# Kernel tuning notes

Hardware: AMD Instinct MI355X
Metric: run time of the kernel (lower is better)

Reference implementation:

```python
import jax, jax.numpy as jnp
import numpy as np

DIM = 1024
HEADS = 16
DIM_HEAD = 64
INNER = HEADS * DIM_HEAD  # 1024
SCALE = DIM_HEAD ** -0.5


def setup_inputs() -> dict:
    key = jax.random.key(0)
    k1, k2, k3, k4 = jax.random.split(key, 4)
    B, N = 2, 2048
    x = jax.random.normal(k1, (B, N, DIM), dtype=jnp.float32)
    # to_qkv: Linear(dim, 3*inner_dim, bias=False); weight stored as [out, in] in torch,
    # here as [in, out] for x @ W.
    w_qkv = jax.random.normal(k2, (DIM, 3 * INNER), dtype=jnp.float32) * (DIM ** -0.5)
    # to_out: Linear(inner_dim, dim) with bias
    w_out = jax.random.normal(k3, (INNER, DIM), dtype=jnp.float32) * (INNER ** -0.5)
    b_out = jax.random.normal(k4, (DIM,), dtype=jnp.float32) * 0.02
    return {"x": x, "w_qkv": w_qkv, "w_out": w_out, "b_out": b_out}


def reference(x, w_qkv, w_out, b_out):
    B, N, _ = x.shape
    qkv = x @ w_qkv                                  # [B, N, 3*INNER]
    q, k, v = jnp.split(qkv, 3, axis=-1)             # each [B, N, INNER]
    def to_heads(t):
        return t.reshape(B, N, HEADS, DIM_HEAD).transpose(0, 2, 1, 3)  # [B,H,N,D]
    q, k, v = to_heads(q), to_heads(k), to_heads(v)
    dots = jnp.einsum('bhnd,bhmd->bhnm', q, k) * SCALE  # [B,H,N,N]
    attn = jax.nn.softmax(dots, axis=-1)
    out = jnp.einsum('bhnm,bhmd->bhnd', attn, v)        # [B,H,N,D]
    out = out.transpose(0, 2, 1, 3).reshape(B, N, INNER)
    return out @ w_out + b_out
```

## Files before the change

### kernel.cpp

```cpp
#include <hip/hip_runtime.h>
#include <hip/hip_bf16.h>
#include <stdint.h>

#define PDIM   1024
#define HEADS  16
#define DHEAD  64
#define BATCH  2
#define SEQ    2048
#define ROWS   (BATCH*SEQ)
#define NBH    (BATCH*HEADS)

typedef __attribute__((ext_vector_type(8))) short s8v;
typedef __attribute__((ext_vector_type(4))) float f32x4;
typedef __attribute__((ext_vector_type(16))) float f32x16;
typedef unsigned short ushort_t;
typedef unsigned int   uint32;

#define QSCALE 0.18033688011112042f
#define MFIX 12.0f

__device__ __forceinline__ ushort_t f2bf(float x){
  union { float f; uint32 u; } v; v.f = x;
  uint32 r = v.u + 0x7FFFu + ((v.u >> 16) & 1u);
  return (ushort_t)(r >> 16);
}
__device__ __forceinline__ uint32 cvt_pk_bf16(float lo, float hi){
  uint32 r;
  asm("v_cvt_pk_bf16_f32 %0, %1, %2" : "=v"(r) : "v"(lo), "v"(hi));
  return r;
}

typedef const __attribute__((address_space(1))) void* gas_ptr;
typedef __attribute__((address_space(3))) void*       las_ptr;
__device__ __forceinline__ void g2l16(const void* g, void* l){
  __builtin_amdgcn_global_load_lds((gas_ptr)g, (las_ptr)l, 16, 0, 0);
}

__global__ __launch_bounds__(256) void k_prep(
    const float* __restrict__ x, const float* __restrict__ w_qkv,
    const float* __restrict__ w_out,
    ushort_t* __restrict__ Xh, ushort_t* __restrict__ Wqt_h,
    ushort_t* __restrict__ Wot_h){
  __shared__ float tile[64][65];
  const int bid = blockIdx.x;
  if (bid < 4096){
    int i = bid * 256 + threadIdx.x;
    float4 v = reinterpret_cast<const float4*>(x)[i];
    reinterpret_cast<ushort4*>(Xh)[i] =
        make_ushort4(f2bf(v.x), f2bf(v.y), f2bf(v.z), f2bf(v.w));
    return;
  }
  const float* src; ushort_t* dst; int R, C, cb, rb;
  if (bid < 4864){
    int t = bid - 4096; src = w_qkv; dst = Wqt_h; R = 1024; C = 3072;
    cb = (t % 48) * 64; rb = (t / 48) * 64;
  } else {
    int t = bid - 4864; src = w_out; dst = Wot_h; R = 1024; C = 1024;
    cb = (t % 16) * 64; rb = (t / 16) * 64;
  }
  int t = threadIdx.x;
  int lw = t >> 6, lc = t & 63;
#pragma unroll
  for (int i = 0; i < 16; i++){
    int r = i * 4 + lw;
    tile[r][lc] = src[(size_t)(rb + r) * C + cb + lc];
  }
  __syncthreads();
#pragma unroll
  for (int i = 0; i < 16; i++){
    int c = i * 4 + lw;
    dst[(size_t)(cb + c) * R + rb + lc] = f2bf(tile[lc][c]);
  }
}

#define GBM 128
#define GBN 128
#define GBK 64

__global__ __launch_bounds__(256, 2) void k_gemm_qkv(
    const ushort_t* __restrict__ Xh, const ushort_t* __restrict__ Wqt_h,
    ushort_t* __restrict__ Qh, ushort_t* __restrict__ Kh, ushort_t* __restrict__ Vth){
  __shared__ __align__(16) ushort_t Asm[2][GBM * GBK];
  __shared__ __align__(16) ushort_t Bsm[2][GBM * GBK];
  const int tid  = threadIdx.x;
  const int wave = tid >> 6, lane = tid & 63;
  const int mb = blockIdx.y * GBM, nb = blockIdx.x * GBN;
  const int wr = wave >> 1, wc = wave & 1;
  const int l15 = lane & 15, l4 = lane >> 4;
  const int rsub = lane >> 3;
  const int schunk = ((lane & 7) ^ rsub) * 8;
  f32x4 acc[4][4] = {};

  auto stage = [&](int buf, int kb){
    int k0 = kb * GBK;
#pragma unroll
    for (int i = 0; i < 4; i++){
      int row = (i * 4 + wave) * 8 + rsub;
      g2l16(Xh    + (size_t)(mb + row) * 1024 + k0 + schunk, &Asm[buf][(i * 4 + wave) * 512]);
      g2l16(Wqt_h + (size_t)(nb + row) * 1024 + k0 + schunk, &Bsm[buf][(i * 4 + wave) * 512]);
    }
  };

  stage(0, 0);

  for (int kb = 0; kb < 16; kb++){
    const int cur = kb & 1;
    if (kb < 15){
      stage(cur ^ 1, kb + 1);
      asm volatile("s_waitcnt vmcnt(8)" ::: "memory");
    } else {
      asm volatile("s_waitcnt vmcnt(0)" ::: "memory");
    }
    __builtin_amdgcn_s_barrier();
    __builtin_amdgcn_s_setprio(1);
#pragma unroll
    for (int ks = 0; ks < 2; ks++){
      s8v af[4], bfr[4];
#pragma unroll
      for (int f = 0; f < 4; f++){
        int ch = (((ks * 4 + l4) ^ (l15 & 7)) << 3);
        af[f]  = *reinterpret_cast<const s8v*>(&Asm[cur][(wr * 64 + f * 16 + l15) * 64 + ch]);
        bfr[f] = *reinterpret_cast<const s8v*>(&Bsm[cur][(wc * 64 + f * 16 + l15) * 64 + ch]);
      }
#pragma unroll
      for (int fr = 0; fr < 4; fr++)
#pragma unroll
        for (int fc = 0; fc < 4; fc++)
          acc[fr][fc] = __builtin_amdgcn_mfma_f32_16x16x32_bf16(af[fr], bfr[fc], acc[fr][fc], 0, 0, 0);
    }
    __builtin_amdgcn_s_setprio(0);
    __builtin_amdgcn_s_barrier();
  }

  const int pnum = nb >> 10;
#pragma unroll
  for (int fr = 0; fr < 4; fr++){
    int row  = mb + wr * 64 + fr * 16 + l4 * 4;
    int b    = row >> 11;
    int nseq = row & 2047;
#pragma unroll
    for (int fc = 0; fc < 4; fc++){
      int col = nb + wc * 64 + fc * 16 + l15;
      int rem = col & 1023;
      int h = rem >> 6, d = rem & 63;
      int bh = b * 16 + h;
      if (pnum == 0){
        size_t base = ((size_t)bh * SEQ + nseq) * 64 + d;
#pragma unroll
        for (int r = 0; r < 4; r++)
          Qh[base + (size_t)r * 64] = f2bf(acc[fr][fc][r] * QSCALE);
      } else if (pnum == 1){
        size_t base = ((size_t)bh * SEQ + nseq) * 64 + d;
#pragma unroll
        for (int r = 0; r < 4; r++)
          Kh[base + (size_t)r * 64] = f2bf(acc[fr][fc][r]);
      } else {
        size_t base = ((size_t)bh * 64 + d) * SEQ + nseq;
        *reinterpret_cast<ushort4*>(&Vth[base]) =
            make_ushort4(f2bf(acc[fr][fc][0]), f2bf(acc[fr][fc][1]),
                         f2bf(acc[fr][fc][2]), f2bf(acc[fr][fc][3]));
      }
    }
  }
}

__global__ __launch_bounds__(256, 2) void k_gemm_out(
    const ushort_t* __restrict__ Ah, const ushort_t* __restrict__ Bth,
    float* __restrict__ C, const float* __restrict__ bias){
  __shared__ __align__(16) ushort_t Asm[2][GBM * GBK];
  __shared__ __align__(16) ushort_t Bsm[2][GBM * GBK];
  const int tid  = threadIdx.x;
  const int wave = tid >> 6, lane = tid & 63;
  const int mb = blockIdx.y * GBM, nb = blockIdx.x * GBN;
  const int wr = wave >> 1, wc = wave & 1;
  const int l15 = lane & 15, l4 = lane >> 4;
  const int rsub = lane >> 3;
  const int schunk = ((lane & 7) ^ rsub) * 8;
  f32x4 acc[4][4] = {};

  auto stage = [&](int buf, int kb){
    int k0 = kb * GBK;
#pragma unroll
    for (int i = 0; i < 4; i++){
      int row = (i * 4 + wave) * 8 + rsub;
      g2l16(Ah  + (size_t)(mb + row) * 1024 + k0 + schunk, &Asm[buf][(i * 4 + wave) * 512]);
      g2l16(Bth + (size_t)(nb + row) * 1024 + k0 + schunk, &Bsm[buf][(i * 4 + wave) * 512]);
    }
  };

  stage(0, 0);

  for (int kb = 0; kb < 16; kb++){
    const int cur = kb & 1;
    if (kb < 15){
      stage(cur ^ 1, kb + 1);
      asm volatile("s_waitcnt vmcnt(8)" ::: "memory");
    } else {
      asm volatile("s_waitcnt vmcnt(0)" ::: "memory");
    }
    __builtin_amdgcn_s_barrier();
    __builtin_amdgcn_s_setprio(1);
#pragma unroll
    for (int ks = 0; ks < 2; ks++){
      s8v af[4], bfr[4];
#pragma unroll
      for (int f = 0; f < 4; f++){
        int ch = (((ks * 4 + l4) ^ (l15 & 7)) << 3);
        af[f]  = *reinterpret_cast<const s8v*>(&Asm[cur][(wr * 64 + f * 16 + l15) * 64 + ch]);
        bfr[f] = *reinterpret_cast<const s8v*>(&Bsm[cur][(wc * 64 + f * 16 + l15) * 64 + ch]);
      }
#pragma unroll
      for (int fr = 0; fr < 4; fr++)
#pragma unroll
        for (int fc = 0; fc < 4; fc++)
          acc[fr][fc] = __builtin_amdgcn_mfma_f32_16x16x32_bf16(af[fr], bfr[fc], acc[fr][fc], 0, 0, 0);
    }
    __builtin_amdgcn_s_setprio(0);
    __builtin_amdgcn_s_barrier();
  }
#pragma unroll
  for (int fr = 0; fr < 4; fr++){
    int row = mb + wr * 64 + fr * 16 + l4 * 4;
#pragma unroll
    for (int fc = 0; fc < 4; fc++){
      int col = nb + wc * 64 + fc * 16 + l15;
      float bv = bias[col];
#pragma unroll
      for (int r = 0; r < 4; r++)
        C[(size_t)(row + r) * 1024 + col] = acc[fr][fc][r] + bv;
    }
  }
}

__global__ __launch_bounds__(256, 2) void k_flash(
    const ushort_t* __restrict__ Qh, const ushort_t* __restrict__ Kh,
    const ushort_t* __restrict__ Vth, ushort_t* __restrict__ Ah){
  __shared__ __align__(16) ushort_t KhS[2][64 * 64];
  __shared__ __align__(16) ushort_t VhS[2][64 * 64];
  const int lid = blockIdx.x;
  const int xcd = lid & 7, g = lid >> 3;
  const int bh = xcd * 4 + (g & 3);
  const int qb = (g >> 2) * 128;
  const int tid = threadIdx.x, wave = tid >> 6, lane = tid & 63;
  const int l31 = lane & 31, hh = lane >> 5;
  const int b = bh >> 4, hd = bh & 15;
  const size_t hbase = (size_t)bh * SEQ * 64;
  const int rsub = lane >> 3;
  const int schunk = ((lane & 7) ^ rsub) * 8;

  int fch[4];
#pragma unroll
  for (int s = 0; s < 4; s++)
    fch[s] = (((2 * s + hh) ^ (l31 & 7)) << 3);
  const int fbase = l31 * 64;

  s8v qf[4];
#pragma unroll
  for (int s = 0; s < 4; s++)
    qf[s] = *reinterpret_cast<const s8v*>(
        &Qh[hbase + (size_t)(qb + wave * 32 + l31) * 64 + s * 16 + hh * 8]);

  f32x16 o0 = {}, o1 = {};
  float lsum = 0.f;

  auto stage = [&](int buf, int kt){
    int kvb = kt * 64;
#pragma unroll
    for (int i = 0; i < 2; i++){
      int row = (i * 4 + wave) * 8 + rsub;
      g2l16(Kh  + hbase + (size_t)(kvb + row) * 64 + schunk, &KhS[buf][(i * 4 + wave) * 512]);
      g2l16(Vth + ((size_t)bh * 64 + row) * SEQ + kvb + schunk, &VhS[buf][(i * 4 + wave) * 512]);
    }
  };

  stage(0, 0);

  for (int kt = 0; kt < 32; kt++){
    const int cur = kt & 1;
    if (kt < 31){
      stage(cur ^ 1, kt + 1);
      asm volatile("s_waitcnt vmcnt(4)" ::: "memory");
    } else {
      asm volatile("s_waitcnt vmcnt(0)" ::: "memory");
    }
    __builtin_amdgcn_s_barrier();

    f32x16 s0 = {}, s1 = {};
    __builtin_amdgcn_s_setprio(1);
#pragma unroll
    for (int s = 0; s < 4; s++){
      s8v kf0 = *reinterpret_cast<const s8v*>(&KhS[cur][fbase + fch[s]]);
      s8v kf1 = *reinterpret_cast<const s8v*>(&KhS[cur][fbase + 2048 + fch[s]]);
      s0 = __builtin_amdgcn_mfma_f32_32x32x16_bf16(kf0, qf[s], s0, 0, 0, 0);
      s1 = __builtin_amdgcn_mfma_f32_32x32x16_bf16(kf1, qf[s], s1, 0, 0, 0);
    }
    __builtin_amdgcn_s_setprio(0);

    uint32 w[2][8];
#pragma unroll
    for (int t = 0; t < 8; t++){
      float pa = __builtin_amdgcn_exp2f(s0[2 * t]     - MFIX);
      float pb = __builtin_amdgcn_exp2f(s0[2 * t + 1] - MFIX);
      lsum += pa + pb;
      w[0][t] = cvt_pk_bf16(pa, pb);
    }
#pragma unroll
    for (int t = 0; t < 8; t++){
      float pa = __builtin_amdgcn_exp2f(s1[2 * t]     - MFIX);
      float pb = __builtin_amdgcn_exp2f(s1[2 * t + 1] - MFIX);
      lsum += pa + pb;
      w[1][t] = cvt_pk_bf16(pa, pb);
    }

    __builtin_amdgcn_s_setprio(1);
#pragma unroll
    for (int s = 0; s < 4; s++){
      const int rb = s >> 1, u = (s & 1) * 4;
      uint32 m0 = w[rb][u],     m2 = w[rb][u + 2];
      uint32 m1 = w[rb][u + 1], m3 = w[rb][u + 3];
      asm("v_permlane32_swap_b32 %0, %1" : "+v"(m0), "+v"(m2));
      asm("v_permlane32_swap_b32 %0, %1" : "+v"(m1), "+v"(m3));
      union { uint32 u4[4]; s8v v; } pf;
      pf.u4[0] = m0; pf.u4[1] = m1; pf.u4[2] = m2; pf.u4[3] = m3;
      s8v vf0 = *reinterpret_cast<const s8v*>(&VhS[cur][fbase + fch[s]]);
      s8v vf1 = *reinterpret_cast<const s8v*>(&VhS[cur][fbase + 2048 + fch[s]]);
      o0 = __builtin_amdgcn_mfma_f32_32x32x16_bf16(pf.v, vf0, o0, 0, 0, 0);
      o1 = __builtin_amdgcn_mfma_f32_32x32x16_bf16(pf.v, vf1, o1, 0, 0, 0);
    }
    __builtin_amdgcn_s_setprio(0);
    __builtin_amdgcn_s_barrier();
  }

  lsum += __shfl_xor(lsum, 32);
  float linv = 1.f / lsum;
#pragma unroll
  for (int r = 0; r < 16; r++){
    int q = (r & 3) + 8 * (r >> 2) + 4 * hh;
    float sc = __shfl(linv, q);
    int n = qb + wave * 32 + q;
    size_t rowb = (size_t)(b * SEQ + n) * 1024 + hd * 64;
    Ah[rowb + l31]      = f2bf(o0[r] * sc);
    Ah[rowb + 32 + l31] = f2bf(o1[r] * sc);
  }
}

extern "C" void kernel_launch(void* const* d_in, const int* in_sizes, int n_in,
                              void* d_out, int out_size, void* d_ws, size_t ws_size,
                              hipStream_t stream){
  const float* x     = (const float*)d_in[0];
  const float* w_qkv = (const float*)d_in[1];
  const float* w_out = (const float*)d_in[2];
  const float* b_out = (const float*)d_in[3];
  float* out = (float*)d_out;
  char* ws = (char*)d_ws;

  ushort_t* Xh    = (ushort_t*)(ws);
  ushort_t* Wqt_h = (ushort_t*)(ws + 8388608);
  ushort_t* Wot_h = (ushort_t*)(ws + 14680064);
  ushort_t* Qh    = (ushort_t*)(ws + 16777216);
  ushort_t* Kh    = (ushort_t*)(ws + 25165824);
  ushort_t* Vth   = (ushort_t*)(ws + 33554432);
  ushort_t* Ah    = (ushort_t*)(ws + 41943040);

  k_prep<<<5120, 256, 0, stream>>>(x, w_qkv, w_out, Xh, Wqt_h, Wot_h);
  k_gemm_qkv<<<dim3(24, 32), 256, 0, stream>>>(Xh, Wqt_h, Qh, Kh, Vth);
  k_flash<<<512, 256, 0, stream>>>(Qh, Kh, Vth, Ah);
  k_gemm_out<<<dim3(8, 32), 256, 0, stream>>>(Ah, Wot_h, out, b_out);
}
```

Before: 115.7 us.

## Shrink flash tiles to 64 queries and 32 keys with 2-wave blocks

The flash-attention kernel now runs 2-wave blocks of 64 query rows and iterates over 32-key tiles (64 steps instead of 32). The grid doubles to 1024 blocks and LDS per block halves, allowing more resident blocks per CU. A new V-tile swizzle and pointer-increment staging are added. Separately, the Q softmax scale is folded into the transposed Q weights in the prep kernel instead of being applied in the QKV GEMM epilogue. The trade-off is more barriers and K/V loads per query row, which lowers data reuse.

```diff
diff --git a/kernel.cpp b/kernel.cpp
--- a/kernel.cpp
+++ b/kernel.cpp
@@ -51,9 +51,11 @@
     return;
   }
   const float* src; ushort_t* dst; int R, C, cb, rb;
+  float scl = 1.f;
   if (bid < 4864){
     int t = bid - 4096; src = w_qkv; dst = Wqt_h; R = 1024; C = 3072;
     cb = (t % 48) * 64; rb = (t / 48) * 64;
+    if (cb < 1024) scl = QSCALE;
   } else {
     int t = bid - 4864; src = w_out; dst = Wot_h; R = 1024; C = 1024;
     cb = (t % 16) * 64; rb = (t / 16) * 64;
@@ -69,7 +71,7 @@
 #pragma unroll
   for (int i = 0; i < 16; i++){
     int c = i * 4 + lw;
-    dst[(size_t)(cb + c) * R + rb + lc] = f2bf(tile[lc][c]);
+    dst[(size_t)(cb + c) * R + rb + lc] = f2bf(tile[lc][c] * scl);
   }
 }
 
@@ -148,7 +150,7 @@
         size_t base = ((size_t)bh * SEQ + nseq) * 64 + d;
 #pragma unroll
         for (int r = 0; r < 4; r++)
-          Qh[base + (size_t)r * 64] = f2bf(acc[fr][fc][r] * QSCALE);
+          Qh[base + (size_t)r * 64] = f2bf(acc[fr][fc][r]);
       } else if (pnum == 1){
         size_t base = ((size_t)bh * SEQ + nseq) * 64 + d;
 #pragma unroll
@@ -232,27 +234,30 @@
   }
 }
 
-__global__ __launch_bounds__(256, 2) void k_flash(
+__global__ __launch_bounds__(128, 4) void k_flash(
     const ushort_t* __restrict__ Qh, const ushort_t* __restrict__ Kh,
     const ushort_t* __restrict__ Vth, ushort_t* __restrict__ Ah){
-  __shared__ __align__(16) ushort_t KhS[2][64 * 64];
-  __shared__ __align__(16) ushort_t VhS[2][64 * 64];
+  __shared__ __align__(16) ushort_t KhS[2][32 * 64];
+  __shared__ __align__(16) ushort_t VhS[2][64 * 32];
   const int lid = blockIdx.x;
   const int xcd = lid & 7, g = lid >> 3;
   const int bh = xcd * 4 + (g & 3);
-  const int qb = (g >> 2) * 128;
+  const int qb = (g >> 2) * 64;
   const int tid = threadIdx.x, wave = tid >> 6, lane = tid & 63;
   const int l31 = lane & 31, hh = lane >> 5;
   const int b = bh >> 4, hd = bh & 15;
   const size_t hbase = (size_t)bh * SEQ * 64;
   const int rsub = lane >> 3;
-  const int schunk = ((lane & 7) ^ rsub) * 8;
-
-  int fch[4];
-#pragma unroll
-  for (int s = 0; s < 4; s++)
-    fch[s] = (((2 * s + hh) ^ (l31 & 7)) << 3);
-  const int fbase = l31 * 64;
+  const int schunkK = ((lane & 7) ^ rsub) * 8;
+  const int schunkV = ((lane & 3) ^ ((lane >> 2) & 3)) * 8;
+
+  int fchK[4], fchV[2];
+#pragma unroll
+  for (int s = 0; s < 4; s++) fchK[s] = (((2 * s + hh) ^ (l31 & 7)) << 3);
+#pragma unroll
+  for (int s = 0; s < 2; s++) fchV[s] = (((2 * s + hh) ^ (l31 & 3)) << 3);
+  const int fbK = l31 * 64;
+  const int fbV = l31 * 32;
 
   s8v qf[4];
 #pragma unroll
@@ -263,67 +268,60 @@
   f32x16 o0 = {}, o1 = {};
   float lsum = 0.f;
 
-  auto stage = [&](int buf, int kt){
-    int kvb = kt * 64;
-#pragma unroll
-    for (int i = 0; i < 2; i++){
-      int row = (i * 4 + wave) * 8 + rsub;
-      g2l16(Kh  + hbase + (size_t)(kvb + row) * 64 + schunk, &KhS[buf][(i * 4 + wave) * 512]);
-      g2l16(Vth + ((size_t)bh * 64 + row) * SEQ + kvb + schunk, &VhS[buf][(i * 4 + wave) * 512]);
-    }
+  const ushort_t* kp0 = Kh + hbase + (size_t)(wave * 8 + rsub) * 64 + schunkK;
+  const ushort_t* kp1 = kp0 + (size_t)16 * 64;
+  const ushort_t* vp0 = Vth + ((size_t)bh * 64 + wave * 16 + (lane >> 2)) * SEQ + schunkV;
+  const ushort_t* vp1 = vp0 + (size_t)32 * SEQ;
+
+  auto stage = [&](int buf){
+    g2l16(kp0, &KhS[buf][wave * 512]);        kp0 += 2048;
+    g2l16(kp1, &KhS[buf][1024 + wave * 512]); kp1 += 2048;
+    g2l16(vp0, &VhS[buf][wave * 512]);        vp0 += 32;
+    g2l16(vp1, &VhS[buf][1024 + wave * 512]); vp1 += 32;
   };
 
-  stage(0, 0);
-
-  for (int kt = 0; kt < 32; kt++){
+  stage(0);
+
+  for (int kt = 0; kt < 64; kt++){
     const int cur = kt & 1;
-    if (kt < 31){
-      stage(cur ^ 1, kt + 1);
+    if (kt < 63){
+      stage(cur ^ 1);
       asm volatile("s_waitcnt vmcnt(4)" ::: "memory");
     } else {
       asm volatile("s_waitcnt vmcnt(0)" ::: "memory");
     }
     __builtin_amdgcn_s_barrier();
 
-    f32x16 s0 = {}, s1 = {};
+    f32x16 s0 = {};
     __builtin_amdgcn_s_setprio(1);
 #pragma unroll
     for (int s = 0; s < 4; s++){
-      s8v kf0 = *reinterpret_cast<const s8v*>(&KhS[cur][fbase + fch[s]]);
-      s8v kf1 = *reinterpret_cast<const s8v*>(&KhS[cur][fbase + 2048 + fch[s]]);
-      s0 = __builtin_amdgcn_mfma_f32_32x32x16_bf16(kf0, qf[s], s0, 0, 0, 0);
-      s1 = __builtin_amdgcn_mfma_f32_32x32x16_bf16(kf1, qf[s], s1, 0, 0, 0);
+      s8v kf = *reinterpret_cast<const s8v*>(&KhS[cur][fbK + fchK[s]]);
+      s0 = __builtin_amdgcn_mfma_f32_32x32x16_bf16(kf, qf[s], s0, 0, 0, 0);
     }
     __builtin_amdgcn_s_setprio(0);
 
-    uint32 w[2][8];
+    uint32 w[8];
 #pragma unroll
     for (int t = 0; t < 8; t++){
       float pa = __builtin_amdgcn_exp2f(s0[2 * t]     - MFIX);
       float pb = __builtin_amdgcn_exp2f(s0[2 * t + 1] - MFIX);
       lsum += pa + pb;
-      w[0][t] = cvt_pk_bf16(pa, pb);
-    }
-#pragma unroll
-    for (int t = 0; t < 8; t++){
-      float pa = __builtin_amdgcn_exp2f(s1[2 * t]     - MFIX);
-      float pb = __builtin_amdgcn_exp2f(s1[2 * t + 1] - MFIX);
-      lsum += pa + pb;
-      w[1][t] = cvt_pk_bf16(pa, pb);
+      w[t] = cvt_pk_bf16(pa, pb);
     }
 
     __builtin_amdgcn_s_setprio(1);
 #pragma unroll
-    for (int s = 0; s < 4; s++){
-      const int rb = s >> 1, u = (s & 1) * 4;
-      uint32 m0 = w[rb][u],     m2 = w[rb][u + 2];
-      uint32 m1 = w[rb][u + 1], m3 = w[rb][u + 3];
+    for (int s = 0; s < 2; s++){
+      const int u = 4 * s;
+      uint32 m0 = w[u],     m2 = w[u + 2];
+      uint32 m1 = w[u + 1], m3 = w[u + 3];
       asm("v_permlane32_swap_b32 %0, %1" : "+v"(m0), "+v"(m2));
       asm("v_permlane32_swap_b32 %0, %1" : "+v"(m1), "+v"(m3));
       union { uint32 u4[4]; s8v v; } pf;
       pf.u4[0] = m0; pf.u4[1] = m1; pf.u4[2] = m2; pf.u4[3] = m3;
-      s8v vf0 = *reinterpret_cast<const s8v*>(&VhS[cur][fbase + fch[s]]);
-      s8v vf1 = *reinterpret_cast<const s8v*>(&VhS[cur][fbase + 2048 + fch[s]]);
+      s8v vf0 = *reinterpret_cast<const s8v*>(&VhS[cur][fbV + fchV[s]]);
+      s8v vf1 = *reinterpret_cast<const s8v*>(&VhS[cur][fbV + 1024 + fchV[s]]);
       o0 = __builtin_amdgcn_mfma_f32_32x32x16_bf16(pf.v, vf0, o0, 0, 0, 0);
       o1 = __builtin_amdgcn_mfma_f32_32x32x16_bf16(pf.v, vf1, o1, 0, 0, 0);
     }
@@ -364,6 +362,6 @@
 
   k_prep<<<5120, 256, 0, stream>>>(x, w_qkv, w_out, Xh, Wqt_h, Wot_h);
   k_gemm_qkv<<<dim3(24, 32), 256, 0, stream>>>(Xh, Wqt_h, Qh, Kh, Vth);
-  k_flash<<<512, 256, 0, stream>>>(Qh, Kh, Vth, Ah);
+  k_flash<<<1024, 128, 0, stream>>>(Qh, Kh, Vth, Ah);
   k_gemm_out<<<dim3(8, 32), 256, 0, stream>>>(Ah, Wot_h, out, b_out);
 }
```

Result: slower. 134.0 us (+15.8%).

## Split flash attention over KV halves with a combine kernel and fold Q scale into weights

Applied to the files above, without the earlier changes.

The attention kernel now splits the KV range in two, launching twice as many blocks. Each block writes unnormalised fp32 partial outputs and row sums, and a new combine kernel adds the halves, normalises, and writes bf16 output. This works because a fixed max offset is used, so no rescaling is needed. The Q scale is folded into the bf16 conversion of the Q weight columns in the prep kernel, and the occupancy hints for the QKV GEMM and attention kernels are raised. The aim is more parallelism and occupancy across the GPU. The cost is extra fp32 traffic and one more kernel launch.

```diff
diff --git a/kernel.cpp b/kernel.cpp
--- a/kernel.cpp
+++ b/kernel.cpp
@@ -51,9 +51,11 @@
     return;
   }
   const float* src; ushort_t* dst; int R, C, cb, rb;
+  float scl = 1.f;
   if (bid < 4864){
     int t = bid - 4096; src = w_qkv; dst = Wqt_h; R = 1024; C = 3072;
     cb = (t % 48) * 64; rb = (t / 48) * 64;
+    if (cb < 1024) scl = QSCALE;
   } else {
     int t = bid - 4864; src = w_out; dst = Wot_h; R = 1024; C = 1024;
     cb = (t % 16) * 64; rb = (t / 16) * 64;
@@ -69,7 +71,7 @@
 #pragma unroll
   for (int i = 0; i < 16; i++){
     int c = i * 4 + lw;
-    dst[(size_t)(cb + c) * R + rb + lc] = f2bf(tile[lc][c]);
+    dst[(size_t)(cb + c) * R + rb + lc] = f2bf(tile[lc][c] * scl);
   }
 }
 
@@ -77,7 +79,7 @@
 #define GBN 128
 #define GBK 64
 
-__global__ __launch_bounds__(256, 2) void k_gemm_qkv(
+__global__ __launch_bounds__(256, 3) void k_gemm_qkv(
     const ushort_t* __restrict__ Xh, const ushort_t* __restrict__ Wqt_h,
     ushort_t* __restrict__ Qh, ushort_t* __restrict__ Kh, ushort_t* __restrict__ Vth){
   __shared__ __align__(16) ushort_t Asm[2][GBM * GBK];
@@ -148,7 +150,7 @@
         size_t base = ((size_t)bh * SEQ + nseq) * 64 + d;
 #pragma unroll
         for (int r = 0; r < 4; r++)
-          Qh[base + (size_t)r * 64] = f2bf(acc[fr][fc][r] * QSCALE);
+          Qh[base + (size_t)r * 64] = f2bf(acc[fr][fc][r]);
       } else if (pnum == 1){
         size_t base = ((size_t)bh * SEQ + nseq) * 64 + d;
 #pragma unroll
@@ -232,18 +234,20 @@
   }
 }
 
-__global__ __launch_bounds__(256, 2) void k_flash(
+__global__ __launch_bounds__(256, 4) void k_flash(
     const ushort_t* __restrict__ Qh, const ushort_t* __restrict__ Kh,
-    const ushort_t* __restrict__ Vth, ushort_t* __restrict__ Ah){
+    const ushort_t* __restrict__ Vth, float* __restrict__ Of, float* __restrict__ Lf){
   __shared__ __align__(16) ushort_t KhS[2][64 * 64];
   __shared__ __align__(16) ushort_t VhS[2][64 * 64];
   const int lid = blockIdx.x;
   const int xcd = lid & 7, g = lid >> 3;
   const int bh = xcd * 4 + (g & 3);
-  const int qb = (g >> 2) * 128;
+  const int rest = g >> 2;
+  const int qb = (rest & 15) * 128;
+  const int sp = rest >> 4;
+  const int kt0 = sp * 16;
   const int tid = threadIdx.x, wave = tid >> 6, lane = tid & 63;
   const int l31 = lane & 31, hh = lane >> 5;
-  const int b = bh >> 4, hd = bh & 15;
   const size_t hbase = (size_t)bh * SEQ * 64;
   const int rsub = lane >> 3;
   const int schunk = ((lane & 7) ^ rsub) * 8;
@@ -260,6 +264,7 @@
     qf[s] = *reinterpret_cast<const s8v*>(
         &Qh[hbase + (size_t)(qb + wave * 32 + l31) * 64 + s * 16 + hh * 8]);
 
+  const f32x16 fzero = {};
   f32x16 o0 = {}, o1 = {};
   float lsum = 0.f;
 
@@ -273,26 +278,29 @@
     }
   };
 
-  stage(0, 0);
-
-  for (int kt = 0; kt < 32; kt++){
-    const int cur = kt & 1;
-    if (kt < 31){
-      stage(cur ^ 1, kt + 1);
+  stage(0, kt0);
+
+  for (int i = 0; i < 16; i++){
+    const int cur = i & 1;
+    if (i < 15){
+      stage(cur ^ 1, kt0 + i + 1);
       asm volatile("s_waitcnt vmcnt(4)" ::: "memory");
     } else {
       asm volatile("s_waitcnt vmcnt(0)" ::: "memory");
     }
     __builtin_amdgcn_s_barrier();
 
-    f32x16 s0 = {}, s1 = {};
     __builtin_amdgcn_s_setprio(1);
-#pragma unroll
-    for (int s = 0; s < 4; s++){
-      s8v kf0 = *reinterpret_cast<const s8v*>(&KhS[cur][fbase + fch[s]]);
-      s8v kf1 = *reinterpret_cast<const s8v*>(&KhS[cur][fbase + 2048 + fch[s]]);
-      s0 = __builtin_amdgcn_mfma_f32_32x32x16_bf16(kf0, qf[s], s0, 0, 0, 0);
-      s1 = __builtin_amdgcn_mfma_f32_32x32x16_bf16(kf1, qf[s], s1, 0, 0, 0);
+    s8v kf0 = *reinterpret_cast<const s8v*>(&KhS[cur][fbase + fch[0]]);
+    s8v kg0 = *reinterpret_cast<const s8v*>(&KhS[cur][fbase + 2048 + fch[0]]);
+    f32x16 s0 = __builtin_amdgcn_mfma_f32_32x32x16_bf16(kf0, qf[0], fzero, 0, 0, 0);
+    f32x16 s1 = __builtin_amdgcn_mfma_f32_32x32x16_bf16(kg0, qf[0], fzero, 0, 0, 0);
+#pragma unroll
+    for (int s = 1; s < 4; s++){
+      s8v kf = *reinterpret_cast<const s8v*>(&KhS[cur][fbase + fch[s]]);
+      s8v kg = *reinterpret_cast<const s8v*>(&KhS[cur][fbase + 2048 + fch[s]]);
+      s0 = __builtin_amdgcn_mfma_f32_32x32x16_bf16(kf, qf[s], s0, 0, 0, 0);
+      s1 = __builtin_amdgcn_mfma_f32_32x32x16_bf16(kg, qf[s], s1, 0, 0, 0);
     }
     __builtin_amdgcn_s_setprio(0);
 
@@ -332,16 +340,37 @@
   }
 
   lsum += __shfl_xor(lsum, 32);
-  float linv = 1.f / lsum;
+  const size_t obase = (size_t)(sp * 32 + bh) * 2048;
+  if (hh == 0)
+    Lf[obase + qb + wave * 32 + l31] = lsum;
 #pragma unroll
   for (int r = 0; r < 16; r++){
     int q = (r & 3) + 8 * (r >> 2) + 4 * hh;
-    float sc = __shfl(linv, q);
     int n = qb + wave * 32 + q;
-    size_t rowb = (size_t)(b * SEQ + n) * 1024 + hd * 64;
-    Ah[rowb + l31]      = f2bf(o0[r] * sc);
-    Ah[rowb + 32 + l31] = f2bf(o1[r] * sc);
-  }
+    size_t rowb = (obase + n) * 64;
+    Of[rowb + l31]      = o0[r];
+    Of[rowb + 32 + l31] = o1[r];
+  }
+}
+
+__global__ __launch_bounds__(256) void k_comb(
+    const float* __restrict__ Of, const float* __restrict__ Lf,
+    ushort_t* __restrict__ Ah){
+  const int bid = blockIdx.x;
+  const int bh = bid >> 7;
+  const int idx = (bid & 127) * 256 + threadIdx.x;
+  const int q = idx >> 4;
+  const int dd = (idx & 15) << 2;
+  const size_t base = ((size_t)bh * 2048 + q) * 64 + dd;
+  float4 a0 = *reinterpret_cast<const float4*>(&Of[base]);
+  float4 a1 = *reinterpret_cast<const float4*>(&Of[base + (size_t)NBH * 2048 * 64]);
+  float L = Lf[(size_t)bh * 2048 + q] + Lf[(size_t)(32 + bh) * 2048 + q];
+  float inv = 1.f / L;
+  int b = bh >> 4, h = bh & 15;
+  size_t orow = ((size_t)(b * 2048 + q)) * 1024 + h * 64 + dd;
+  *reinterpret_cast<ushort4*>(&Ah[orow]) =
+      make_ushort4(f2bf((a0.x + a1.x) * inv), f2bf((a0.y + a1.y) * inv),
+                   f2bf((a0.z + a1.z) * inv), f2bf((a0.w + a1.w) * inv));
 }
 
 extern "C" void kernel_launch(void* const* d_in, const int* in_sizes, int n_in,
@@ -361,9 +390,12 @@
   ushort_t* Kh    = (ushort_t*)(ws + 25165824);
   ushort_t* Vth   = (ushort_t*)(ws + 33554432);
   ushort_t* Ah    = (ushort_t*)(ws + 41943040);
+  float*    Of    = (float*)(ws + 50331648);
+  float*    Lf    = (float*)(ws + 83886080);
 
   k_prep<<<5120, 256, 0, stream>>>(x, w_qkv, w_out, Xh, Wqt_h, Wot_h);
   k_gemm_qkv<<<dim3(24, 32), 256, 0, stream>>>(Xh, Wqt_h, Qh, Kh, Vth);
-  k_flash<<<512, 256, 0, stream>>>(Qh, Kh, Vth, Ah);
+  k_flash<<<1024, 256, 0, stream>>>(Qh, Kh, Vth, Of, Lf);
+  k_comb<<<4096, 256, 0, stream>>>(Of, Lf, Ah);
   k_gemm_out<<<dim3(8, 32), 256, 0, stream>>>(Ah, Wot_h, out, b_out);
 }
```

After: 125.8 us. 1.09x slower.

## Give each flash wave two query groups, halve block threads, fold Q scale into weights

Applied to the files above, without the earlier changes.

The flash kernel now runs 128 threads per block, with each wave handling 64 query rows as two 32-row groups. Every K/V fragment read from shared memory feeds twice as many MFMAs, which cuts LDS traffic per FLOP but raises register pressure (four score accumulators plus four output accumulators). The Q softmax scale moves into the weight preparation step, so the QKV GEMM epilogue no longer multiplies. The QKV GEMM launch bound also asks for three blocks per CU instead of two.

```diff
diff --git a/kernel.cpp b/kernel.cpp
--- a/kernel.cpp
+++ b/kernel.cpp
@@ -51,9 +51,11 @@
     return;
   }
   const float* src; ushort_t* dst; int R, C, cb, rb;
+  float scl = 1.f;
   if (bid < 4864){
     int t = bid - 4096; src = w_qkv; dst = Wqt_h; R = 1024; C = 3072;
     cb = (t % 48) * 64; rb = (t / 48) * 64;
+    if (cb < 1024) scl = QSCALE;
   } else {
     int t = bid - 4864; src = w_out; dst = Wot_h; R = 1024; C = 1024;
     cb = (t % 16) * 64; rb = (t / 16) * 64;
@@ -69,7 +71,7 @@
 #pragma unroll
   for (int i = 0; i < 16; i++){
     int c = i * 4 + lw;
-    dst[(size_t)(cb + c) * R + rb + lc] = f2bf(tile[lc][c]);
+    dst[(size_t)(cb + c) * R + rb + lc] = f2bf(tile[lc][c] * scl);
   }
 }
 
@@ -77,7 +79,7 @@
 #define GBN 128
 #define GBK 64
 
-__global__ __launch_bounds__(256, 2) void k_gemm_qkv(
+__global__ __launch_bounds__(256, 3) void k_gemm_qkv(
     const ushort_t* __restrict__ Xh, const ushort_t* __restrict__ Wqt_h,
     ushort_t* __restrict__ Qh, ushort_t* __restrict__ Kh, ushort_t* __restrict__ Vth){
   __shared__ __align__(16) ushort_t Asm[2][GBM * GBK];
@@ -148,7 +150,7 @@
         size_t base = ((size_t)bh * SEQ + nseq) * 64 + d;
 #pragma unroll
         for (int r = 0; r < 4; r++)
-          Qh[base + (size_t)r * 64] = f2bf(acc[fr][fc][r] * QSCALE);
+          Qh[base + (size_t)r * 64] = f2bf(acc[fr][fc][r]);
       } else if (pnum == 1){
         size_t base = ((size_t)bh * SEQ + nseq) * 64 + d;
 #pragma unroll
@@ -232,7 +234,7 @@
   }
 }
 
-__global__ __launch_bounds__(256, 2) void k_flash(
+__global__ __launch_bounds__(128, 2) void k_flash(
     const ushort_t* __restrict__ Qh, const ushort_t* __restrict__ Kh,
     const ushort_t* __restrict__ Vth, ushort_t* __restrict__ Ah){
   __shared__ __align__(16) ushort_t KhS[2][64 * 64];
@@ -254,22 +256,25 @@
     fch[s] = (((2 * s + hh) ^ (l31 & 7)) << 3);
   const int fbase = l31 * 64;
 
-  s8v qf[4];
-#pragma unroll
-  for (int s = 0; s < 4; s++)
-    qf[s] = *reinterpret_cast<const s8v*>(
-        &Qh[hbase + (size_t)(qb + wave * 32 + l31) * 64 + s * 16 + hh * 8]);
-
-  f32x16 o0 = {}, o1 = {};
-  float lsum = 0.f;
+  s8v qf[2][4];
+#pragma unroll
+  for (int grp = 0; grp < 2; grp++)
+#pragma unroll
+    for (int s = 0; s < 4; s++)
+      qf[grp][s] = *reinterpret_cast<const s8v*>(
+          &Qh[hbase + (size_t)(qb + wave * 64 + grp * 32 + l31) * 64 + s * 16 + hh * 8]);
+
+  const f32x16 fzero = {};
+  f32x16 o[2][2] = {};
+  float lsum[2] = {0.f, 0.f};
 
   auto stage = [&](int buf, int kt){
     int kvb = kt * 64;
 #pragma unroll
-    for (int i = 0; i < 2; i++){
-      int row = (i * 4 + wave) * 8 + rsub;
-      g2l16(Kh  + hbase + (size_t)(kvb + row) * 64 + schunk, &KhS[buf][(i * 4 + wave) * 512]);
-      g2l16(Vth + ((size_t)bh * 64 + row) * SEQ + kvb + schunk, &VhS[buf][(i * 4 + wave) * 512]);
+    for (int i = 0; i < 4; i++){
+      int row = (i * 2 + wave) * 8 + rsub;
+      g2l16(Kh  + hbase + (size_t)(kvb + row) * 64 + schunk, &KhS[buf][(i * 2 + wave) * 512]);
+      g2l16(Vth + ((size_t)bh * 64 + row) * SEQ + kvb + schunk, &VhS[buf][(i * 2 + wave) * 512]);
     }
   };
 
@@ -279,68 +284,79 @@
     const int cur = kt & 1;
     if (kt < 31){
       stage(cur ^ 1, kt + 1);
-      asm volatile("s_waitcnt vmcnt(4)" ::: "memory");
+      asm volatile("s_waitcnt vmcnt(8)" ::: "memory");
     } else {
       asm volatile("s_waitcnt vmcnt(0)" ::: "memory");
     }
     __builtin_amdgcn_s_barrier();
 
-    f32x16 s0 = {}, s1 = {};
+    f32x16 s00 = fzero, s01 = fzero, s10 = fzero, s11 = fzero;
     __builtin_amdgcn_s_setprio(1);
 #pragma unroll
     for (int s = 0; s < 4; s++){
       s8v kf0 = *reinterpret_cast<const s8v*>(&KhS[cur][fbase + fch[s]]);
       s8v kf1 = *reinterpret_cast<const s8v*>(&KhS[cur][fbase + 2048 + fch[s]]);
-      s0 = __builtin_amdgcn_mfma_f32_32x32x16_bf16(kf0, qf[s], s0, 0, 0, 0);
-      s1 = __builtin_amdgcn_mfma_f32_32x32x16_bf16(kf1, qf[s], s1, 0, 0, 0);
+      s00 = __builtin_amdgcn_mfma_f32_32x32x16_bf16(kf0, qf[0][s], s00, 0, 0, 0);
+      s01 = __builtin_amdgcn_mfma_f32_32x32x16_bf16(kf1, qf[0][s], s01, 0, 0, 0);
+      s10 = __builtin_amdgcn_mfma_f32_32x32x16_bf16(kf0, qf[1][s], s10, 0, 0, 0);
+      s11 = __builtin_amdgcn_mfma_f32_32x32x16_bf16(kf1, qf[1][s], s11, 0, 0, 0);
     }
     __builtin_amdgcn_s_setprio(0);
 
-    uint32 w[2][8];
+    uint32 w[2][2][8];
 #pragma unroll
     for (int t = 0; t < 8; t++){
-      float pa = __builtin_amdgcn_exp2f(s0[2 * t]     - MFIX);
-      float pb = __builtin_amdgcn_exp2f(s0[2 * t + 1] - MFIX);
-      lsum += pa + pb;
-      w[0][t] = cvt_pk_bf16(pa, pb);
-    }
-#pragma unroll
-    for (int t = 0; t < 8; t++){
-      float pa = __builtin_amdgcn_exp2f(s1[2 * t]     - MFIX);
-      float pb = __builtin_amdgcn_exp2f(s1[2 * t + 1] - MFIX);
-      lsum += pa + pb;
-      w[1][t] = cvt_pk_bf16(pa, pb);
+      float a0 = __builtin_amdgcn_exp2f(s00[2 * t]     - MFIX);
+      float b0 = __builtin_amdgcn_exp2f(s00[2 * t + 1] - MFIX);
+      float a1 = __builtin_amdgcn_exp2f(s01[2 * t]     - MFIX);
+      float b1 = __builtin_amdgcn_exp2f(s01[2 * t + 1] - MFIX);
+      lsum[0] += (a0 + b0) + (a1 + b1);
+      w[0][0][t] = cvt_pk_bf16(a0, b0);
+      w[0][1][t] = cvt_pk_bf16(a1, b1);
+      float a2 = __builtin_amdgcn_exp2f(s10[2 * t]     - MFIX);
+      float b2 = __builtin_amdgcn_exp2f(s10[2 * t + 1] - MFIX);
+      float a3 = __builtin_amdgcn_exp2f(s11[2 * t]     - MFIX);
+      float b3 = __builtin_amdgcn_exp2f(s11[2 * t + 1] - MFIX);
+      lsum[1] += (a2 + b2) + (a3 + b3);
+      w[1][0][t] = cvt_pk_bf16(a2, b2);
+      w[1][1][t] = cvt_pk_bf16(a3, b3);
     }
 
     __builtin_amdgcn_s_setprio(1);
 #pragma unroll
-    for (int s = 0; s < 4; s++){
-      const int rb = s >> 1, u = (s & 1) * 4;
-      uint32 m0 = w[rb][u],     m2 = w[rb][u + 2];
-      uint32 m1 = w[rb][u + 1], m3 = w[rb][u + 3];
-      asm("v_permlane32_swap_b32 %0, %1" : "+v"(m0), "+v"(m2));
-      asm("v_permlane32_swap_b32 %0, %1" : "+v"(m1), "+v"(m3));
-      union { uint32 u4[4]; s8v v; } pf;
-      pf.u4[0] = m0; pf.u4[1] = m1; pf.u4[2] = m2; pf.u4[3] = m3;
-      s8v vf0 = *reinterpret_cast<const s8v*>(&VhS[cur][fbase + fch[s]]);
-      s8v vf1 = *reinterpret_cast<const s8v*>(&VhS[cur][fbase + 2048 + fch[s]]);
-      o0 = __builtin_amdgcn_mfma_f32_32x32x16_bf16(pf.v, vf0, o0, 0, 0, 0);
-      o1 = __builtin_amdgcn_mfma_f32_32x32x16_bf16(pf.v, vf1, o1, 0, 0, 0);
+    for (int st = 0; st < 4; st++){
+      const int rb = st >> 1, u = (st & 1) * 4;
+      s8v vf0 = *reinterpret_cast<const s8v*>(&VhS[cur][fbase + fch[st]]);
+      s8v vf1 = *reinterpret_cast<const s8v*>(&VhS[cur][fbase + 2048 + fch[st]]);
+#pragma unroll
+      for (int grp = 0; grp < 2; grp++){
+        uint32 m0 = w[grp][rb][u],     m2 = w[grp][rb][u + 2];
+        uint32 m1 = w[grp][rb][u + 1], m3 = w[grp][rb][u + 3];
+        asm("v_permlane32_swap_b32 %0, %1" : "+v"(m0), "+v"(m2));
+        asm("v_permlane32_swap_b32 %0, %1" : "+v"(m1), "+v"(m3));
+        union { uint32 u4[4]; s8v v; } pf;
+        pf.u4[0] = m0; pf.u4[1] = m1; pf.u4[2] = m2; pf.u4[3] = m3;
+        o[grp][0] = __builtin_amdgcn_mfma_f32_32x32x16_bf16(pf.v, vf0, o[grp][0], 0, 0, 0);
+        o[grp][1] = __builtin_amdgcn_mfma_f32_32x32x16_bf16(pf.v, vf1, o[grp][1], 0, 0, 0);
+      }
     }
     __builtin_amdgcn_s_setprio(0);
     __builtin_amdgcn_s_barrier();
   }
 
-  lsum += __shfl_xor(lsum, 32);
-  float linv = 1.f / lsum;
-#pragma unroll
-  for (int r = 0; r < 16; r++){
-    int q = (r & 3) + 8 * (r >> 2) + 4 * hh;
-    float sc = __shfl(linv, q);
-    int n = qb + wave * 32 + q;
-    size_t rowb = (size_t)(b * SEQ + n) * 1024 + hd * 64;
-    Ah[rowb + l31]      = f2bf(o0[r] * sc);
-    Ah[rowb + 32 + l31] = f2bf(o1[r] * sc);
+#pragma unroll
+  for (int grp = 0; grp < 2; grp++){
+    float ls = lsum[grp] + __shfl_xor(lsum[grp], 32);
+    float linv = 1.f / ls;
+#pragma unroll
+    for (int r = 0; r < 16; r++){
+      int q = (r & 3) + 8 * (r >> 2) + 4 * hh;
+      float sc = __shfl(linv, q);
+      int n = qb + wave * 64 + grp * 32 + q;
+      size_t rowb = (size_t)(b * SEQ + n) * 1024 + hd * 64;
+      Ah[rowb + l31]      = f2bf(o[grp][0][r] * sc);
+      Ah[rowb + 32 + l31] = f2bf(o[grp][1][r] * sc);
+    }
   }
 }
 
@@ -364,6 +380,6 @@
 
   k_prep<<<5120, 256, 0, stream>>>(x, w_qkv, w_out, Xh, Wqt_h, Wot_h);
   k_gemm_qkv<<<dim3(24, 32), 256, 0, stream>>>(Xh, Wqt_h, Qh, Kh, Vth);
-  k_flash<<<512, 256, 0, stream>>>(Qh, Kh, Vth, Ah);
+  k_flash<<<512, 128, 0, stream>>>(Qh, Kh, Vth, Ah);
   k_gemm_out<<<dim3(8, 32), 256, 0, stream>>>(Ah, Wot_h, out, b_out);
 }
```

Result: slower. 144.3 us (+24.7%).
